# Optimization experiments

Hardware: AMD Instinct MI355X
Metric: run time of the kernel (lower is better)

The kernel has to match this reference:

```python
import jax, jax.numpy as jnp
import numpy as np

P, N, NF = 4, 871, 512            # num_meta_paths, node_size (hardcoded 871 in source), node_feature_size
XDIM = 116 * 116                   # x_proj input dim, hardcoded Linear(116*116, nf)
BETA, LAMBDA_WL, GAMMA = 0.1, 0.1, 0.1


def _xavier(k, shape):
    fan_in, fan_out = shape[0], shape[-1]
    bound = np.sqrt(6.0 / (fan_in + fan_out))
    return jax.random.uniform(k, shape, jnp.float32, -bound, bound)


def setup_inputs() -> dict:
    key = jax.random.key(0)
    ks = jax.random.split(key, 12)
    return {
        "z_stack": jax.random.normal(ks[0], (P, N, NF), jnp.float32),
        "x_orig": jax.random.normal(ks[1], (1, 116, 116), jnp.float32),
        "W": _xavier(ks[2], (N, 1)),
        "b": jax.random.uniform(ks[3], (N, 1), jnp.float32),
        "q": _xavier(ks[4], (N, NF)),
        "xp_w": _xavier(ks[5], (XDIM, NF)),
        "xp_b": jnp.zeros((NF,), jnp.float32),
        "w1": _xavier(ks[6], (2 * NF, 512)), "b1": jnp.zeros((512,), jnp.float32),
        "w2": _xavier(ks[7], (512, 256)), "b2": jnp.zeros((256,), jnp.float32),
        "w3": _xavier(ks[8], (256, 1)), "b3": jnp.zeros((1,), jnp.float32),
        "perm": jax.random.permutation(ks[9], N).astype(jnp.int32),
    }


def _mi_mlp(t, w1, b1, w2, b2, w3, b3):
    h = jax.nn.relu(t @ w1 + b1)
    h = jax.nn.relu(h @ w2 + b2)
    return h @ w3 + b3  # [N, 1]


def reference(z_stack, x_orig, W, b, q, xp_w, xp_b, w1, b1, w2, b2, w3, b3, perm):
    # --- vectorized form of the per-node loop:
    # score_p = mean_i( tanh(W_i * z[p,i,:] + b_i) . q_i )
    zt = jnp.tanh(W[None] * z_stack + b[None])            # [P,N,NF]
    scores = jnp.mean(jnp.sum(zt * q[None], axis=-1), axis=-1)  # [P]
    proportions = scores / jnp.sum(scores)
    attn = jax.nn.softmax(proportions)                    # [P] (no isomorphic pairs -> no overwrite)
    # layer_out_p = attn_p * z_p + z_p ; emb = sum_p layer_out_p
    emb = jnp.einsum('p,pnf->nf', 1.0 + attn, z_stack)    # [N,NF]
    # --- estimate_MI(x_orig, emb, mi_estimator_xz)
    x = jnp.broadcast_to(x_orig.reshape(1, -1), (N, XDIM))
    xh = x @ xp_w + xp_b                                  # [N,NF]
    t0 = jnp.concatenate([xh, emb], axis=1)               # [N,2NF]
    t1 = jnp.concatenate([xh, emb[perm]], axis=1)
    mi_lb = jnp.mean(_mi_mlp(t0, w1, b1, w2, b2, w3, b3)) - jnp.log(
        jnp.mean(jnp.exp(_mi_mlp(t1, w1, b1, w2, b2, w3, b3))) + 1e-8)
    I_XZ = jnp.clip(mi_lb, 0.0)
    # y_labels=None -> I_ZY = 0 ; empty isomorphic_pairs -> wl_loss = 0
    total_loss = I_XZ - BETA * 0.0 + LAMBDA_WL * 0.0 + GAMMA * jnp.sum(attn)
    return emb, total_loss
```

## Files before the change

### kernel.cpp

```cpp
#include <hip/hip_runtime.h>
#include <hip/hip_bf16.h>
#include <math.h>

#define NMETA  4
#define NNODE  871
#define NFEAT  512
#define XDIM   (116*116)
#define ZPLANE (NNODE*NFEAT)
#define Z4     (ZPLANE/4)
#define NCHUNK 55
#define MPAD   896
#define MT     56

#define WS_SPART  16
#define WS_C1P    256
#define WS_E1     8448
#define WS_XHP    WS_E1
#define WS_EMBB   467200
#define WS_V      696576
#define WS_W1P    697448
#define WS_W2P    828520

typedef short v8s __attribute__((ext_vector_type(8)));
typedef float v4f __attribute__((ext_vector_type(4)));

static __device__ __forceinline__ short f2bf(float f) {
  __hip_bfloat16 h = __float2bfloat16(f);
  return *reinterpret_cast<short*>(&h);
}

__global__ __launch_bounds__(256) void k_front(const float* __restrict__ x,
                                               const float* __restrict__ xpw,
                                               const float* __restrict__ w1,
                                               const float* __restrict__ w2,
                                               const float* __restrict__ z,
                                               const float* __restrict__ W,
                                               const float* __restrict__ b,
                                               const float* __restrict__ q,
                                               float* __restrict__ ws,
                                               short* __restrict__ w1p,
                                               short* __restrict__ w2p) {
  const int blk = blockIdx.x;
  const int tid = threadIdx.x;
  if (blk < 128) {
    const int f4 = tid & 127;
    const int rp = tid >> 7;
    const int d0 = blk * 106;
    const int rows = min(106, XDIM - d0);
    __shared__ float xs[106];
    if (tid < rows) xs[tid] = x[d0 + tid];
    __syncthreads();
    float4 acc = {0.f, 0.f, 0.f, 0.f};
    const float4* xp4 = (const float4*)xpw;
#pragma unroll 4
    for (int r = rp; r < rows; r += 2) {
      const float xv = xs[r];
      const float4 w = xp4[(size_t)(d0 + r) * 128 + f4];
      acc.x += xv * w.x; acc.y += xv * w.y; acc.z += xv * w.z; acc.w += xv * w.w;
    }
    __shared__ float4 red4[128];
    if (rp) red4[f4] = acc;
    __syncthreads();
    if (!rp) {
      float4 o = red4[f4];
      o.x += acc.x; o.y += acc.y; o.z += acc.z; o.w += acc.w;
      ((float4*)(ws + WS_XHP + (size_t)blk * NFEAT))[f4] = o;
    }
  } else if (blk < 128 + 1536) {
    int t = (blk - 128) * 256 + tid;
    if (t < 512 * 512) {
      int j = t & 7; int r = t >> 3;
      int n15 = r & 15; r >>= 4;
      int quad = r & 3; r >>= 2;
      int nt = r & 31; int kb = r >> 5;
      int k = kb * 32 + quad * 8 + j;
      int n = nt * 16 + n15;
      w1p[t] = f2bf(w1[(size_t)(512 + k) * 512 + n]);
    } else {
      int o = t - 512 * 512;
      int j = o & 7; int r = o >> 3;
      int n15 = r & 15; r >>= 4;
      int quad = r & 3; r >>= 2;
      int nt = r & 15; int kb = r >> 4;
      int k = kb * 32 + quad * 8 + j;
      int n = nt * 16 + n15;
      w2p[o] = f2bf(w2[(size_t)k * 256 + n]);
    }
  } else {
    const int sblk = blk - 1664;
    const int p = sblk / NCHUNK;
    const int chunk = sblk % NCHUNK;
    const int i0 = chunk * 16;
    const int i1 = min(i0 + 16, NNODE);
    const int f4 = tid & 127;
    const int ip = tid >> 7;
    float local = 0.f;
    for (int i = i0 + ip; i < i1; i += 2) {
      const float wi = W[i];
      const float bi = b[i];
      const float4 zr = ((const float4*)(z + ((size_t)p * NNODE + i) * NFEAT))[f4];
      const float4 qr = ((const float4*)(q + (size_t)i * NFEAT))[f4];
      local += tanhf(wi * zr.x + bi) * qr.x + tanhf(wi * zr.y + bi) * qr.y
             + tanhf(wi * zr.z + bi) * qr.z + tanhf(wi * zr.w + bi) * qr.w;
    }
    __shared__ float red[256];
    red[tid] = local;
    __syncthreads();
    for (int s = 128; s > 0; s >>= 1) {
      if (tid < s) red[tid] += red[tid + s];
      __syncthreads();
    }
    if (tid == 0) ws[WS_SPART + sblk] = red[0];
  }
}

__global__ __launch_bounds__(256) void k_mid(const float* __restrict__ z,
                                             float* __restrict__ ws,
                                             float* __restrict__ emb_out,
                                             short* __restrict__ embb,
                                             const float* __restrict__ xpb,
                                             const float* __restrict__ w1,
                                             const float* __restrict__ b1) {
  const int tid = threadIdx.x;
  if (blockIdx.x < 448) {
    __shared__ float sp[220];
    __shared__ float sc[NMETA];
    if (tid < 220) sp[tid] = ws[WS_SPART + tid];
    __syncthreads();
    if (tid < NMETA) {
      float s = 0.f;
      for (int c = 0; c < NCHUNK; ++c) s += sp[tid * NCHUNK + c];
      sc[tid] = s;
    }
    __syncthreads();
    float sv[NMETA], sum = 0.f;
#pragma unroll
    for (int p = 0; p < NMETA; ++p) { sv[p] = sc[p] / (float)NNODE; sum += sv[p]; }
    float m = -1e30f;
#pragma unroll
    for (int p = 0; p < NMETA; ++p) { sv[p] = sv[p] / sum; m = fmaxf(m, sv[p]); }
    float es = 0.f;
#pragma unroll
    for (int p = 0; p < NMETA; ++p) { sv[p] = expf(sv[p] - m); es += sv[p]; }
    float coef[NMETA];
#pragma unroll
    for (int p = 0; p < NMETA; ++p) coef[p] = 1.f + sv[p] / es;

    const int idx = blockIdx.x * 256 + tid;
    if (idx < Z4) {
      const float4* z4 = (const float4*)z;
      float4 a = z4[idx];
      float4 bb = z4[Z4 + idx];
      float4 c = z4[2 * Z4 + idx];
      float4 d = z4[3 * Z4 + idx];
      float4 r;
      r.x = coef[0] * a.x + coef[1] * bb.x + coef[2] * c.x + coef[3] * d.x;
      r.y = coef[0] * a.y + coef[1] * bb.y + coef[2] * c.y + coef[3] * d.y;
      r.z = coef[0] * a.z + coef[1] * bb.z + coef[2] * c.z + coef[3] * d.z;
      r.w = coef[0] * a.w + coef[1] * bb.w + coef[2] * c.w + coef[3] * d.w;
      ((float4*)emb_out)[idx] = r;
      short4 h;
      h.x = f2bf(r.x); h.y = f2bf(r.y); h.z = f2bf(r.z); h.w = f2bf(r.w);
      ((short4*)embb)[idx] = h;
    } else {
      short4 zr = {0, 0, 0, 0};
      ((short4*)embb)[idx] = zr;
    }
  } else {
    const int bk = blockIdx.x - 448;
    for (int t = tid; t < NCHUNK; t += 256) {
      int vi = bk * NCHUNK + t;
      if (vi < NNODE) ws[WS_V + vi] = 0.f;
    }
    __shared__ float xs[32];
    {
      const int f = tid & 31;
      const int pg = tid >> 5;
      float s = 0.f;
#pragma unroll 4
      for (int p = pg; p < 128; p += 8)
        s += ws[WS_XHP + (size_t)p * NFEAT + bk * 32 + f];
      __shared__ float red[256];
      red[tid] = s;
      __syncthreads();
      if (tid < 32) {
        float t2 = 0.f;
#pragma unroll
        for (int g = 0; g < 8; ++g) t2 += red[g * 32 + tid];
        xs[tid] = t2 + xpb[bk * 32 + tid];
      }
      __syncthreads();
    }
    const int j4 = tid & 127;
    const int fp = tid >> 7;
    float4 acc = {0.f, 0.f, 0.f, 0.f};
    const float4* w14 = (const float4*)w1;
#pragma unroll
    for (int ff = 0; ff < 16; ++ff) {
      const int f = bk * 32 + fp * 16 + ff;
      const float xv = xs[fp * 16 + ff];
      const float4 w = w14[(size_t)f * 128 + j4];
      acc.x += xv * w.x; acc.y += xv * w.y; acc.z += xv * w.z; acc.w += xv * w.w;
    }
    __shared__ float4 red2[128];
    if (fp) red2[j4] = acc;
    __syncthreads();
    if (!fp) {
      float4 o = red2[j4];
      o.x += acc.x; o.y += acc.y; o.z += acc.z; o.w += acc.w;
      if (bk == 0) {
        o.x += b1[j4 * 4 + 0]; o.y += b1[j4 * 4 + 1];
        o.z += b1[j4 * 4 + 2]; o.w += b1[j4 * 4 + 3];
      }
      ((float4*)(ws + WS_C1P + (size_t)bk * NFEAT))[j4] = o;
    }
  }
}

__global__ __launch_bounds__(256) void k_gemmE1(const short* __restrict__ embb,
                                                const short* __restrict__ w1p,
                                                float* __restrict__ E1) {
  const int lane = threadIdx.x & 63;
  const int wid = blockIdx.x * 4 + (threadIdx.x >> 6);
  const int n15 = lane & 15, quad = lane >> 4;
  const int mt = wid % MT;
  const int ng = wid / MT;
  const short* A = embb + (size_t)(mt * 16 + n15) * NFEAT + quad * 8;
  const short* Bbase = w1p + (ng * 16 + quad) * 128 + n15 * 8;
  v4f acc0 = {0.f,0.f,0.f,0.f}, acc1 = acc0, acc2 = acc0, acc3 = acc0;
#pragma unroll
  for (int kb = 0; kb < 16; ++kb) {
    v8s a = *(const v8s*)(A + kb * 32);
    const short* Bp = Bbase + (size_t)kb * 16384;
    v8s b0 = *(const v8s*)(Bp);
    v8s b1 = *(const v8s*)(Bp + 512);
    v8s b2 = *(const v8s*)(Bp + 1024);
    v8s b3 = *(const v8s*)(Bp + 1536);
    acc0 = __builtin_amdgcn_mfma_f32_16x16x32_bf16(a, b0, acc0, 0, 0, 0);
    acc1 = __builtin_amdgcn_mfma_f32_16x16x32_bf16(a, b1, acc1, 0, 0, 0);
    acc2 = __builtin_amdgcn_mfma_f32_16x16x32_bf16(a, b2, acc2, 0, 0, 0);
    acc3 = __builtin_amdgcn_mfma_f32_16x16x32_bf16(a, b3, acc3, 0, 0, 0);
  }
  float* C0 = E1 + (size_t)(mt * 16 + quad * 4) * NFEAT + ng * 64 + n15;
#pragma unroll
  for (int r = 0; r < 4; ++r) {
    C0[(size_t)r * NFEAT +  0] = acc0[r];
    C0[(size_t)r * NFEAT + 16] = acc1[r];
    C0[(size_t)r * NFEAT + 32] = acc2[r];
    C0[(size_t)r * NFEAT + 48] = acc3[r];
  }
}

__global__ __launch_bounds__(256) void k_gemmH2v(const float* __restrict__ E1,
                                                 const float* __restrict__ c1p,
                                                 const short* __restrict__ w2p,
                                                 const float* __restrict__ b2,
                                                 const float* __restrict__ w3,
                                                 float* __restrict__ v) {
  __shared__ float cs[512];
  {
    float a0 = 0.f, a1 = 0.f;
#pragma unroll
    for (int k = 0; k < 16; ++k) {
      a0 += c1p[(size_t)k * 512 + threadIdx.x];
      a1 += c1p[(size_t)k * 512 + 256 + threadIdx.x];
    }
    cs[threadIdx.x] = a0;
    cs[256 + threadIdx.x] = a1;
  }
  __syncthreads();
  const int lane = threadIdx.x & 63;
  const int wid = blockIdx.x * 4 + (threadIdx.x >> 6);
  const int n15 = lane & 15, quad = lane >> 4;
  const int mt = wid % MT;
  const int ng = wid / MT;
  const float* Arow = E1 + (size_t)(mt * 16 + n15) * NFEAT + quad * 8;
  const short* Bbase = w2p + (ng * 16 + quad) * 128 + n15 * 8;
  v4f acc0 = {0.f,0.f,0.f,0.f}, acc1 = acc0, acc2 = acc0, acc3 = acc0;
#pragma unroll
  for (int kb = 0; kb < 16; ++kb) {
    float4 e0 = *(const float4*)(Arow + kb * 32);
    float4 e1 = *(const float4*)(Arow + kb * 32 + 4);
    const float4 ca = *(const float4*)(cs + kb * 32 + quad * 8);
    const float4 cb = *(const float4*)(cs + kb * 32 + quad * 8 + 4);
    v8s a;
    a[0] = f2bf(fmaxf(e0.x + ca.x, 0.f));
    a[1] = f2bf(fmaxf(e0.y + ca.y, 0.f));
    a[2] = f2bf(fmaxf(e0.z + ca.z, 0.f));
    a[3] = f2bf(fmaxf(e0.w + ca.w, 0.f));
    a[4] = f2bf(fmaxf(e1.x + cb.x, 0.f));
    a[5] = f2bf(fmaxf(e1.y + cb.y, 0.f));
    a[6] = f2bf(fmaxf(e1.z + cb.z, 0.f));
    a[7] = f2bf(fmaxf(e1.w + cb.w, 0.f));
    const short* Bp = Bbase + (size_t)kb * 8192;
    v8s b0 = *(const v8s*)(Bp);
    v8s b1 = *(const v8s*)(Bp + 512);
    v8s b2v = *(const v8s*)(Bp + 1024);
    v8s b3 = *(const v8s*)(Bp + 1536);
    acc0 = __builtin_amdgcn_mfma_f32_16x16x32_bf16(a, b0, acc0, 0, 0, 0);
    acc1 = __builtin_amdgcn_mfma_f32_16x16x32_bf16(a, b1, acc1, 0, 0, 0);
    acc2 = __builtin_amdgcn_mfma_f32_16x16x32_bf16(a, b2v, acc2, 0, 0, 0);
    acc3 = __builtin_amdgcn_mfma_f32_16x16x32_bf16(a, b3, acc3, 0, 0, 0);
  }
  const float bb0 = b2[ng * 64 + n15],      bb1 = b2[ng * 64 + 16 + n15];
  const float bb2 = b2[ng * 64 + 32 + n15], bb3 = b2[ng * 64 + 48 + n15];
  const float w30 = w3[ng * 64 + n15],      w31 = w3[ng * 64 + 16 + n15];
  const float w32 = w3[ng * 64 + 32 + n15], w33 = w3[ng * 64 + 48 + n15];
  const int grow0 = mt * 16 + quad * 4;
#pragma unroll
  for (int r = 0; r < 4; ++r) {
    float s = fmaxf(acc0[r] + bb0, 0.f) * w30
            + fmaxf(acc1[r] + bb1, 0.f) * w31
            + fmaxf(acc2[r] + bb2, 0.f) * w32
            + fmaxf(acc3[r] + bb3, 0.f) * w33;
    s += __shfl_xor(s, 1);
    s += __shfl_xor(s, 2);
    s += __shfl_xor(s, 4);
    s += __shfl_xor(s, 8);
    const int grow = grow0 + r;
    if (n15 == 0 && grow < NNODE) atomicAdd(&v[grow], s);
  }
}

__global__ void k_final(const float* __restrict__ ws, const float* __restrict__ b3,
                        float* __restrict__ out) {
  const float* v = ws + WS_V;
  const float bias = b3[0];
  float s0 = 0.f, s1 = 0.f;
  for (int i = threadIdx.x; i < NNODE; i += 256) {
    float x = v[i] + bias;
    s0 += x;
    s1 += expf(x);
  }
  __shared__ float r0[256], r1[256];
  r0[threadIdx.x] = s0; r1[threadIdx.x] = s1;
  __syncthreads();
  for (int s = 128; s > 0; s >>= 1) {
    if ((int)threadIdx.x < s) {
      r0[threadIdx.x] += r0[threadIdx.x + s];
      r1[threadIdx.x] += r1[threadIdx.x + s];
    }
    __syncthreads();
  }
  if (threadIdx.x == 0) {
    float m0 = r0[0] / (float)NNODE;
    float m1 = r1[0] / (float)NNODE;
    float mi = m0 - logf(m1 + 1e-8f);
    out[ZPLANE] = fmaxf(mi, 0.f) + 0.1f;
  }
}

extern "C" void kernel_launch(void* const* d_in, const int* in_sizes, int n_in,
                              void* d_out, int out_size, void* d_ws, size_t ws_size,
                              hipStream_t stream) {
  const float* z   = (const float*)d_in[0];
  const float* x   = (const float*)d_in[1];
  const float* W   = (const float*)d_in[2];
  const float* b   = (const float*)d_in[3];
  const float* q   = (const float*)d_in[4];
  const float* xpw = (const float*)d_in[5];
  const float* xpb = (const float*)d_in[6];
  const float* w1  = (const float*)d_in[7];
  const float* b1  = (const float*)d_in[8];
  const float* w2  = (const float*)d_in[9];
  const float* b2  = (const float*)d_in[10];
  const float* w3  = (const float*)d_in[11];
  const float* b3  = (const float*)d_in[12];
  float* out = (float*)d_out;
  float* ws  = (float*)d_ws;

  short* embb = (short*)(ws + WS_EMBB);
  short* w1p  = (short*)(ws + WS_W1P);
  short* w2p  = (short*)(ws + WS_W2P);

  k_front<<<1884, 256, 0, stream>>>(x, xpw, w1, w2, z, W, b, q, ws, w1p, w2p);
  k_mid<<<464, 256, 0, stream>>>(z, ws, out, embb, xpb, w1, b1);
  k_gemmE1<<<112, 256, 0, stream>>>(embb, w1p, ws + WS_E1);
  k_gemmH2v<<<56, 256, 0, stream>>>(ws + WS_E1, ws + WS_C1P, w2p, b2, w3, ws + WS_V);
  k_final<<<1, 256, 0, stream>>>(ws, b3, out);
}
```

Before: 132.8 us.

## Fuse emb combine, both MLP GEMMs and final reduction into one kernel

Replaces the mid, GEMM and final kernels with a small prep kernel (softmax coefficients, c1 partials, zeroing) and a fused kernel per 16-row tile. Each tile computes emb from z, keeps the bf16 copy in a swizzled LDS buffer, runs both MFMA layers with the hidden activations held in LDS, and finishes the MI reduction via a last-block atomic counter. It also packs the weight conversion into fewer blocks with a four-step loop. This cuts kernel launches and global round trips for emb and E1, but only 55 blocks run the heavy fused stage, so parallelism is low.

```diff
diff --git a/kernel.cpp b/kernel.cpp
--- a/kernel.cpp
+++ b/kernel.cpp
@@ -7,19 +7,17 @@
 #define NFEAT  512
 #define XDIM   (116*116)
 #define ZPLANE (NNODE*NFEAT)
-#define Z4     (ZPLANE/4)
 #define NCHUNK 55
-#define MPAD   896
-#define MT     56
-
+#define MT     55
+
+#define WS_COEF   8
+#define WS_CNT    12
 #define WS_SPART  16
 #define WS_C1P    256
-#define WS_E1     8448
-#define WS_XHP    WS_E1
-#define WS_EMBB   467200
-#define WS_V      696576
-#define WS_W1P    697448
-#define WS_W2P    828520
+#define WS_XHP    8448
+#define WS_V      73984
+#define WS_W1P    74856
+#define WS_W2P    205928
 
 typedef short v8s __attribute__((ext_vector_type(8)));
 typedef float v4f __attribute__((ext_vector_type(4)));
@@ -66,28 +64,32 @@
       o.x += acc.x; o.y += acc.y; o.z += acc.z; o.w += acc.w;
       ((float4*)(ws + WS_XHP + (size_t)blk * NFEAT))[f4] = o;
     }
-  } else if (blk < 128 + 1536) {
-    int t = (blk - 128) * 256 + tid;
-    if (t < 512 * 512) {
-      int j = t & 7; int r = t >> 3;
-      int n15 = r & 15; r >>= 4;
-      int quad = r & 3; r >>= 2;
-      int nt = r & 31; int kb = r >> 5;
-      int k = kb * 32 + quad * 8 + j;
-      int n = nt * 16 + n15;
-      w1p[t] = f2bf(w1[(size_t)(512 + k) * 512 + n]);
-    } else {
-      int o = t - 512 * 512;
-      int j = o & 7; int r = o >> 3;
-      int n15 = r & 15; r >>= 4;
-      int quad = r & 3; r >>= 2;
-      int nt = r & 15; int kb = r >> 4;
-      int k = kb * 32 + quad * 8 + j;
-      int n = nt * 16 + n15;
-      w2p[o] = f2bf(w2[(size_t)k * 256 + n]);
+  } else if (blk < 512) {
+    const int base = (blk - 128) * 256 + tid;
+#pragma unroll
+    for (int it = 0; it < 4; ++it) {
+      int t = base + it * 98304;
+      if (t < 262144) {
+        int j = t & 7; int r = t >> 3;
+        int n15 = r & 15; r >>= 4;
+        int quad = r & 3; r >>= 2;
+        int nt = r & 31; int kb = r >> 5;
+        int k = kb * 32 + quad * 8 + j;
+        int n = nt * 16 + n15;
+        w1p[t] = f2bf(w1[(size_t)(512 + k) * 512 + n]);
+      } else {
+        int o = t - 262144;
+        int j = o & 7; int r = o >> 3;
+        int n15 = r & 15; r >>= 4;
+        int quad = r & 3; r >>= 2;
+        int nt = r & 15; int kb = r >> 4;
+        int k = kb * 32 + quad * 8 + j;
+        int n = nt * 16 + n15;
+        w2p[o] = f2bf(w2[(size_t)k * 256 + n]);
+      }
     }
   } else {
-    const int sblk = blk - 1664;
+    const int sblk = blk - 512;
     const int p = sblk / NCHUNK;
     const int chunk = sblk % NCHUNK;
     const int i0 = chunk * 16;
@@ -114,64 +116,13 @@
   }
 }
 
-__global__ __launch_bounds__(256) void k_mid(const float* __restrict__ z,
-                                             float* __restrict__ ws,
-                                             float* __restrict__ emb_out,
-                                             short* __restrict__ embb,
-                                             const float* __restrict__ xpb,
-                                             const float* __restrict__ w1,
-                                             const float* __restrict__ b1) {
+__global__ __launch_bounds__(256) void k_prep(const float* __restrict__ xpb,
+                                              const float* __restrict__ w1,
+                                              const float* __restrict__ b1,
+                                              float* __restrict__ ws) {
   const int tid = threadIdx.x;
-  if (blockIdx.x < 448) {
-    __shared__ float sp[220];
-    __shared__ float sc[NMETA];
-    if (tid < 220) sp[tid] = ws[WS_SPART + tid];
-    __syncthreads();
-    if (tid < NMETA) {
-      float s = 0.f;
-      for (int c = 0; c < NCHUNK; ++c) s += sp[tid * NCHUNK + c];
-      sc[tid] = s;
-    }
-    __syncthreads();
-    float sv[NMETA], sum = 0.f;
-#pragma unroll
-    for (int p = 0; p < NMETA; ++p) { sv[p] = sc[p] / (float)NNODE; sum += sv[p]; }
-    float m = -1e30f;
-#pragma unroll
-    for (int p = 0; p < NMETA; ++p) { sv[p] = sv[p] / sum; m = fmaxf(m, sv[p]); }
-    float es = 0.f;
-#pragma unroll
-    for (int p = 0; p < NMETA; ++p) { sv[p] = expf(sv[p] - m); es += sv[p]; }
-    float coef[NMETA];
-#pragma unroll
-    for (int p = 0; p < NMETA; ++p) coef[p] = 1.f + sv[p] / es;
-
-    const int idx = blockIdx.x * 256 + tid;
-    if (idx < Z4) {
-      const float4* z4 = (const float4*)z;
-      float4 a = z4[idx];
-      float4 bb = z4[Z4 + idx];
-      float4 c = z4[2 * Z4 + idx];
-      float4 d = z4[3 * Z4 + idx];
-      float4 r;
-      r.x = coef[0] * a.x + coef[1] * bb.x + coef[2] * c.x + coef[3] * d.x;
-      r.y = coef[0] * a.y + coef[1] * bb.y + coef[2] * c.y + coef[3] * d.y;
-      r.z = coef[0] * a.z + coef[1] * bb.z + coef[2] * c.z + coef[3] * d.z;
-      r.w = coef[0] * a.w + coef[1] * bb.w + coef[2] * c.w + coef[3] * d.w;
-      ((float4*)emb_out)[idx] = r;
-      short4 h;
-      h.x = f2bf(r.x); h.y = f2bf(r.y); h.z = f2bf(r.z); h.w = f2bf(r.w);
-      ((short4*)embb)[idx] = h;
-    } else {
-      short4 zr = {0, 0, 0, 0};
-      ((short4*)embb)[idx] = zr;
-    }
-  } else {
-    const int bk = blockIdx.x - 448;
-    for (int t = tid; t < NCHUNK; t += 256) {
-      int vi = bk * NCHUNK + t;
-      if (vi < NNODE) ws[WS_V + vi] = 0.f;
-    }
+  if (blockIdx.x < 16) {
+    const int bk = blockIdx.x;
     __shared__ float xs[32];
     {
       const int f = tid & 31;
@@ -214,139 +165,182 @@
       }
       ((float4*)(ws + WS_C1P + (size_t)bk * NFEAT))[j4] = o;
     }
-  }
-}
-
-__global__ __launch_bounds__(256) void k_gemmE1(const short* __restrict__ embb,
-                                                const short* __restrict__ w1p,
-                                                float* __restrict__ E1) {
-  const int lane = threadIdx.x & 63;
-  const int wid = blockIdx.x * 4 + (threadIdx.x >> 6);
-  const int n15 = lane & 15, quad = lane >> 4;
-  const int mt = wid % MT;
-  const int ng = wid / MT;
-  const short* A = embb + (size_t)(mt * 16 + n15) * NFEAT + quad * 8;
-  const short* Bbase = w1p + (ng * 16 + quad) * 128 + n15 * 8;
-  v4f acc0 = {0.f,0.f,0.f,0.f}, acc1 = acc0, acc2 = acc0, acc3 = acc0;
-#pragma unroll
-  for (int kb = 0; kb < 16; ++kb) {
-    v8s a = *(const v8s*)(A + kb * 32);
-    const short* Bp = Bbase + (size_t)kb * 16384;
-    v8s b0 = *(const v8s*)(Bp);
-    v8s b1 = *(const v8s*)(Bp + 512);
-    v8s b2 = *(const v8s*)(Bp + 1024);
-    v8s b3 = *(const v8s*)(Bp + 1536);
-    acc0 = __builtin_amdgcn_mfma_f32_16x16x32_bf16(a, b0, acc0, 0, 0, 0);
-    acc1 = __builtin_amdgcn_mfma_f32_16x16x32_bf16(a, b1, acc1, 0, 0, 0);
-    acc2 = __builtin_amdgcn_mfma_f32_16x16x32_bf16(a, b2, acc2, 0, 0, 0);
-    acc3 = __builtin_amdgcn_mfma_f32_16x16x32_bf16(a, b3, acc3, 0, 0, 0);
-  }
-  float* C0 = E1 + (size_t)(mt * 16 + quad * 4) * NFEAT + ng * 64 + n15;
-#pragma unroll
-  for (int r = 0; r < 4; ++r) {
-    C0[(size_t)r * NFEAT +  0] = acc0[r];
-    C0[(size_t)r * NFEAT + 16] = acc1[r];
-    C0[(size_t)r * NFEAT + 32] = acc2[r];
-    C0[(size_t)r * NFEAT + 48] = acc3[r];
-  }
-}
-
-__global__ __launch_bounds__(256) void k_gemmH2v(const float* __restrict__ E1,
-                                                 const float* __restrict__ c1p,
-                                                 const short* __restrict__ w2p,
-                                                 const float* __restrict__ b2,
-                                                 const float* __restrict__ w3,
-                                                 float* __restrict__ v) {
+  } else {
+    __shared__ float sp[220];
+    if (tid < 220) sp[tid] = ws[WS_SPART + tid];
+    __syncthreads();
+    if (tid == 0) {
+      float sv[NMETA], sum = 0.f;
+#pragma unroll
+      for (int p = 0; p < NMETA; ++p) {
+        float s = 0.f;
+        for (int c = 0; c < NCHUNK; ++c) s += sp[p * NCHUNK + c];
+        sv[p] = s / (float)NNODE;
+        sum += sv[p];
+      }
+      float m = -1e30f;
+#pragma unroll
+      for (int p = 0; p < NMETA; ++p) { sv[p] = sv[p] / sum; m = fmaxf(m, sv[p]); }
+      float es = 0.f;
+#pragma unroll
+      for (int p = 0; p < NMETA; ++p) { sv[p] = expf(sv[p] - m); es += sv[p]; }
+#pragma unroll
+      for (int p = 0; p < NMETA; ++p) ws[WS_COEF + p] = 1.f + sv[p] / es;
+      *(unsigned int*)&ws[WS_CNT] = 0u;
+    }
+    for (int i = tid; i < NNODE; i += 256) ws[WS_V + i] = 0.f;
+  }
+}
+
+__global__ __launch_bounds__(256) void k_fused(const float* __restrict__ z,
+                                               float* __restrict__ ws,
+                                               float* __restrict__ out,
+                                               const short* __restrict__ w1p,
+                                               const short* __restrict__ w2p,
+                                               const float* __restrict__ b2,
+                                               const float* __restrict__ w3,
+                                               const float* __restrict__ b3) {
+  __shared__ __align__(16) short embs[8192];
+  __shared__ __align__(16) short h2a[8192];
   __shared__ float cs[512];
+  __shared__ float rf0[256], rf1[256];
+  const int tid = threadIdx.x;
+  const int r0 = blockIdx.x * 16;
+
   {
     float a0 = 0.f, a1 = 0.f;
 #pragma unroll
     for (int k = 0; k < 16; ++k) {
-      a0 += c1p[(size_t)k * 512 + threadIdx.x];
-      a1 += c1p[(size_t)k * 512 + 256 + threadIdx.x];
-    }
-    cs[threadIdx.x] = a0;
-    cs[256 + threadIdx.x] = a1;
+      a0 += ws[WS_C1P + k * 512 + tid];
+      a1 += ws[WS_C1P + k * 512 + 256 + tid];
+    }
+    cs[tid] = a0;
+    cs[256 + tid] = a1;
+  }
+  const float c0 = ws[WS_COEF + 0], c1c = ws[WS_COEF + 1];
+  const float c2 = ws[WS_COEF + 2], c3 = ws[WS_COEF + 3];
+
+  const int oc = tid & 63;
+  const float4* z4 = (const float4*)z;
+  float4* out4 = (float4*)out;
+#pragma unroll
+  for (int t = 0; t < 4; ++t) {
+    const int row = (tid >> 6) + 4 * t;
+    const int gr = r0 + row;
+    const int slot = oc * 16 + (row ^ (oc & 15));
+    v8s h;
+    if (gr < NNODE) {
+      const int zi = gr * 128 + oc * 2;
+      float4 a0 = z4[zi],               a1 = z4[zi + 1];
+      float4 b0 = z4[NNODE*128 + zi],   b1 = z4[NNODE*128 + zi + 1];
+      float4 d0 = z4[2*NNODE*128 + zi], d1 = z4[2*NNODE*128 + zi + 1];
+      float4 e0 = z4[3*NNODE*128 + zi], e1 = z4[3*NNODE*128 + zi + 1];
+      float4 r0v, r1v;
+      r0v.x = c0*a0.x + c1c*b0.x + c2*d0.x + c3*e0.x;
+      r0v.y = c0*a0.y + c1c*b0.y + c2*d0.y + c3*e0.y;
+      r0v.z = c0*a0.z + c1c*b0.z + c2*d0.z + c3*e0.z;
+      r0v.w = c0*a0.w + c1c*b0.w + c2*d0.w + c3*e0.w;
+      r1v.x = c0*a1.x + c1c*b1.x + c2*d1.x + c3*e1.x;
+      r1v.y = c0*a1.y + c1c*b1.y + c2*d1.y + c3*e1.y;
+      r1v.z = c0*a1.z + c1c*b1.z + c2*d1.z + c3*e1.z;
+      r1v.w = c0*a1.w + c1c*b1.w + c2*d1.w + c3*e1.w;
+      out4[zi] = r0v;
+      out4[zi + 1] = r1v;
+      h[0] = f2bf(r0v.x); h[1] = f2bf(r0v.y); h[2] = f2bf(r0v.z); h[3] = f2bf(r0v.w);
+      h[4] = f2bf(r1v.x); h[5] = f2bf(r1v.y); h[6] = f2bf(r1v.z); h[7] = f2bf(r1v.w);
+    } else {
+      h = (v8s){0,0,0,0,0,0,0,0};
+    }
+    *(v8s*)(embs + slot * 8) = h;
   }
   __syncthreads();
-  const int lane = threadIdx.x & 63;
-  const int wid = blockIdx.x * 4 + (threadIdx.x >> 6);
+
+  const int lane = tid & 63, w = tid >> 6;
   const int n15 = lane & 15, quad = lane >> 4;
-  const int mt = wid % MT;
-  const int ng = wid / MT;
-  const float* Arow = E1 + (size_t)(mt * 16 + n15) * NFEAT + quad * 8;
-  const short* Bbase = w2p + (ng * 16 + quad) * 128 + n15 * 8;
-  v4f acc0 = {0.f,0.f,0.f,0.f}, acc1 = acc0, acc2 = acc0, acc3 = acc0;
+  v4f e[8];
+#pragma unroll
+  for (int ct = 0; ct < 8; ++ct) e[ct] = (v4f){0.f, 0.f, 0.f, 0.f};
 #pragma unroll
   for (int kb = 0; kb < 16; ++kb) {
-    float4 e0 = *(const float4*)(Arow + kb * 32);
-    float4 e1 = *(const float4*)(Arow + kb * 32 + 4);
-    const float4 ca = *(const float4*)(cs + kb * 32 + quad * 8);
-    const float4 cb = *(const float4*)(cs + kb * 32 + quad * 8 + 4);
-    v8s a;
-    a[0] = f2bf(fmaxf(e0.x + ca.x, 0.f));
-    a[1] = f2bf(fmaxf(e0.y + ca.y, 0.f));
-    a[2] = f2bf(fmaxf(e0.z + ca.z, 0.f));
-    a[3] = f2bf(fmaxf(e0.w + ca.w, 0.f));
-    a[4] = f2bf(fmaxf(e1.x + cb.x, 0.f));
-    a[5] = f2bf(fmaxf(e1.y + cb.y, 0.f));
-    a[6] = f2bf(fmaxf(e1.z + cb.z, 0.f));
-    a[7] = f2bf(fmaxf(e1.w + cb.w, 0.f));
-    const short* Bp = Bbase + (size_t)kb * 8192;
-    v8s b0 = *(const v8s*)(Bp);
-    v8s b1 = *(const v8s*)(Bp + 512);
-    v8s b2v = *(const v8s*)(Bp + 1024);
-    v8s b3 = *(const v8s*)(Bp + 1536);
-    acc0 = __builtin_amdgcn_mfma_f32_16x16x32_bf16(a, b0, acc0, 0, 0, 0);
-    acc1 = __builtin_amdgcn_mfma_f32_16x16x32_bf16(a, b1, acc1, 0, 0, 0);
-    acc2 = __builtin_amdgcn_mfma_f32_16x16x32_bf16(a, b2v, acc2, 0, 0, 0);
-    acc3 = __builtin_amdgcn_mfma_f32_16x16x32_bf16(a, b3, acc3, 0, 0, 0);
-  }
-  const float bb0 = b2[ng * 64 + n15],      bb1 = b2[ng * 64 + 16 + n15];
-  const float bb2 = b2[ng * 64 + 32 + n15], bb3 = b2[ng * 64 + 48 + n15];
-  const float w30 = w3[ng * 64 + n15],      w31 = w3[ng * 64 + 16 + n15];
-  const float w32 = w3[ng * 64 + 32 + n15], w33 = w3[ng * 64 + 48 + n15];
-  const int grow0 = mt * 16 + quad * 4;
+    const int koct = kb * 4 + quad;
+    v8s a = *(const v8s*)(embs + (koct * 16 + (n15 ^ (koct & 15))) * 8);
+    const short* B = w1p + kb * 16384 + w * 4096 + quad * 128 + n15 * 8;
+#pragma unroll
+    for (int ct = 0; ct < 8; ++ct) {
+      v8s bb = *(const v8s*)(B + ct * 512);
+      e[ct] = __builtin_amdgcn_mfma_f32_16x16x32_bf16(a, bb, e[ct], 0, 0, 0);
+    }
+  }
+#pragma unroll
+  for (int ct = 0; ct < 8; ++ct) {
+    const int col = w * 128 + ct * 16 + n15;
+    const int koct = col >> 3, j = col & 7;
+#pragma unroll
+    for (int r = 0; r < 4; ++r) {
+      const int m = quad * 4 + r;
+      h2a[(koct * 16 + (m ^ (koct & 15))) * 8 + j] = f2bf(fmaxf(e[ct][r] + cs[col], 0.f));
+    }
+  }
+  __syncthreads();
+
+  v4f g[4];
+#pragma unroll
+  for (int ct = 0; ct < 4; ++ct) g[ct] = (v4f){0.f, 0.f, 0.f, 0.f};
+#pragma unroll
+  for (int kb = 0; kb < 16; ++kb) {
+    const int koct = kb * 4 + quad;
+    v8s a = *(const v8s*)(h2a + (koct * 16 + (n15 ^ (koct & 15))) * 8);
+    const short* B = w2p + kb * 8192 + w * 2048 + quad * 128 + n15 * 8;
+#pragma unroll
+    for (int ct = 0; ct < 4; ++ct) {
+      v8s bb = *(const v8s*)(B + ct * 512);
+      g[ct] = __builtin_amdgcn_mfma_f32_16x16x32_bf16(a, bb, g[ct], 0, 0, 0);
+    }
+  }
 #pragma unroll
   for (int r = 0; r < 4; ++r) {
-    float s = fmaxf(acc0[r] + bb0, 0.f) * w30
-            + fmaxf(acc1[r] + bb1, 0.f) * w31
-            + fmaxf(acc2[r] + bb2, 0.f) * w32
-            + fmaxf(acc3[r] + bb3, 0.f) * w33;
+    float s = 0.f;
+#pragma unroll
+    for (int ct = 0; ct < 4; ++ct) {
+      const int col = w * 64 + ct * 16 + n15;
+      s += fmaxf(g[ct][r] + b2[col], 0.f) * w3[col];
+    }
     s += __shfl_xor(s, 1);
     s += __shfl_xor(s, 2);
     s += __shfl_xor(s, 4);
     s += __shfl_xor(s, 8);
-    const int grow = grow0 + r;
-    if (n15 == 0 && grow < NNODE) atomicAdd(&v[grow], s);
-  }
-}
-
-__global__ void k_final(const float* __restrict__ ws, const float* __restrict__ b3,
-                        float* __restrict__ out) {
-  const float* v = ws + WS_V;
-  const float bias = b3[0];
-  float s0 = 0.f, s1 = 0.f;
-  for (int i = threadIdx.x; i < NNODE; i += 256) {
-    float x = v[i] + bias;
-    s0 += x;
-    s1 += expf(x);
-  }
-  __shared__ float r0[256], r1[256];
-  r0[threadIdx.x] = s0; r1[threadIdx.x] = s1;
+    const int grow = r0 + quad * 4 + r;
+    if (n15 == 0 && grow < NNODE) atomicAdd(&ws[WS_V + grow], s);
+  }
+
+  __shared__ unsigned last;
   __syncthreads();
-  for (int s = 128; s > 0; s >>= 1) {
-    if ((int)threadIdx.x < s) {
-      r0[threadIdx.x] += r0[threadIdx.x + s];
-      r1[threadIdx.x] += r1[threadIdx.x + s];
-    }
-    __syncthreads();
-  }
-  if (threadIdx.x == 0) {
-    float m0 = r0[0] / (float)NNODE;
-    float m1 = r1[0] / (float)NNODE;
-    float mi = m0 - logf(m1 + 1e-8f);
-    out[ZPLANE] = fmaxf(mi, 0.f) + 0.1f;
+  if (tid == 0) {
+    __threadfence();
+    unsigned old = atomicAdd((unsigned int*)&ws[WS_CNT], 1u);
+    last = (old == MT - 1) ? 1u : 0u;
+  }
+  __syncthreads();
+  if (last) {
+    const float bias = b3[0];
+    float s0 = 0.f, s1 = 0.f;
+    for (int i = tid; i < NNODE; i += 256) {
+      float xv = __hip_atomic_load(&ws[WS_V + i], __ATOMIC_RELAXED, __HIP_MEMORY_SCOPE_AGENT) + bias;
+      s0 += xv;
+      s1 += expf(xv);
+    }
+    rf0[tid] = s0; rf1[tid] = s1;
+    __syncthreads();
+    for (int s = 128; s > 0; s >>= 1) {
+      if (tid < s) { rf0[tid] += rf0[tid + s]; rf1[tid] += rf1[tid + s]; }
+      __syncthreads();
+    }
+    if (tid == 0) {
+      float m0 = rf0[0] / (float)NNODE;
+      float m1 = rf1[0] / (float)NNODE;
+      float mi = m0 - logf(m1 + 1e-8f);
+      out[ZPLANE] = fmaxf(mi, 0.f) + 0.1f;
+    }
   }
 }
 
@@ -369,13 +363,10 @@
   float* out = (float*)d_out;
   float* ws  = (float*)d_ws;
 
-  short* embb = (short*)(ws + WS_EMBB);
-  short* w1p  = (short*)(ws + WS_W1P);
-  short* w2p  = (short*)(ws + WS_W2P);
-
-  k_front<<<1884, 256, 0, stream>>>(x, xpw, w1, w2, z, W, b, q, ws, w1p, w2p);
-  k_mid<<<464, 256, 0, stream>>>(z, ws, out, embb, xpb, w1, b1);
-  k_gemmE1<<<112, 256, 0, stream>>>(embb, w1p, ws + WS_E1);
-  k_gemmH2v<<<56, 256, 0, stream>>>(ws + WS_E1, ws + WS_C1P, w2p, b2, w3, ws + WS_V);
-  k_final<<<1, 256, 0, stream>>>(ws, b3, out);
-}
+  short* w1p = (short*)(ws + WS_W1P);
+  short* w2p = (short*)(ws + WS_W2P);
+
+  k_front<<<732, 256, 0, stream>>>(x, xpw, w1, w2, z, W, b, q, ws, w1p, w2p);
+  k_prep<<<17, 256, 0, stream>>>(xpb, w1, b1, ws);
+  k_fused<<<MT, 256, 0, stream>>>(z, ws, out, w1p, w2p, b2, w3, b3);
+}
```

After: 133.2 us. About the same (+0.3%).
